# Performance work log

Measured on AMD Instinct MI355X. Metric: run time of the kernel, lower is better.

Reference implementation:

```python
import jax, jax.numpy as jnp
import numpy as np

N_SRC, N_DST, N_EDGES, E = 100000, 50000, 600000, 128

def setup_inputs() -> dict:
    key = jax.random.key(0)
    k1, k2, k3, k4, k5, k6 = jax.random.split(key, 6)
    return {
        "h_src": jax.random.normal(k1, (N_SRC, E), dtype=jnp.float32),
        "weights": jax.random.uniform(k2, (N_EDGES,), dtype=jnp.float32),
        "src_idx": jax.random.randint(k3, (N_EDGES,), 0, N_SRC, dtype=jnp.int32),
        "dst_idx": jax.random.randint(k4, (N_EDGES,), 0, N_DST, dtype=jnp.int32),
        "num_dst": N_DST,
        "q_w": jax.random.normal(k5, (E, E), dtype=jnp.float32) * (2.0 / np.sqrt(E + E)),  # xavier-ish, gain=sqrt(2)
        "q_b": jnp.zeros((E,), dtype=jnp.float32),
        "w_w": jax.random.normal(k6, (E, 2 * E), dtype=jnp.float32) * (2.0 / np.sqrt(E + 2 * E)),
        "w_b": jnp.zeros((E,), dtype=jnp.float32),
    }

def reference(h_src, weights, src_idx, dst_idx, num_dst, q_w, q_b, w_w, w_b):
    h_dst = h_src[:num_dst]                                  # [n_dst, E]
    n = jax.nn.relu(h_src @ q_w.T + q_b)                     # [n_src, E] (dropout=eval/no-op)
    w = weights.astype(jnp.float32)
    m = n[src_idx] * w[:, None]                              # [n_edges, E] edge messages
    agg = jax.ops.segment_sum(m, dst_idx, num_segments=num_dst)   # weighted feature sum
    ws = jax.ops.segment_sum(w, dst_idx, num_segments=num_dst)    # weight sum
    ws = jnp.clip(ws, 1.0, None)[:, None]                    # clamp(min=1)
    z = jnp.concatenate([h_dst, agg / ws], axis=1)           # [n_dst, 2E]
    z = jax.nn.relu(z @ w_w.T + w_b)                         # [n_dst, E]
    z_norm = jnp.linalg.norm(z, axis=1, keepdims=True)
    z_norm = jnp.where(z_norm == 0, 1.0, z_norm)
    return z / z_norm
```

## Files before the change

kernel.cpp:

```cpp
#include <hip/hip_runtime.h>
#include <math.h>


typedef __attribute__((ext_vector_type(8))) short  short8;
typedef __attribute__((ext_vector_type(8))) __bf16 bf16x8;
typedef __attribute__((ext_vector_type(4))) float  f32x4;

#define MFMA16(a, b, c) __builtin_amdgcn_mfma_f32_16x16x32_bf16( \
    __builtin_bit_cast(bf16x8, (a)), __builtin_bit_cast(bf16x8, (b)), (c), 0, 0, 0)

#define EDGE_CAP 2048

__device__ __forceinline__ ushort f2bf(float x) {
    unsigned u = __float_as_uint(x);
    return (ushort)((u + 0x7fffu + ((u >> 16) & 1u)) >> 16);
}
__device__ __forceinline__ float bfhi(unsigned p) { return __uint_as_float(p & 0xffff0000u); }
__device__ __forceinline__ float bflo(unsigned p) { return __uint_as_float(p << 16); }

__device__ __forceinline__ short8 cvt8(float4 v0, float4 v1) {
    ushort t[8] = { f2bf(v0.x), f2bf(v0.y), f2bf(v0.z), f2bf(v0.w),
                    f2bf(v1.x), f2bf(v1.y), f2bf(v1.z), f2bf(v1.w) };
    return *(short8*)t;
}

__global__ __launch_bounds__(512) void k_hist(const int* __restrict__ dst,
    int* __restrict__ hist, int nedges, int nb)
{
    __shared__ int hl[2048];
    const int g = blockIdx.x, tid = threadIdx.x, G = gridDim.x;
    for (int i = tid; i < nb; i += 512) hl[i] = 0;
    __syncthreads();
    const int chunk = (nedges + G - 1) / G;
    const int e0 = g * chunk, e1 = min(e0 + chunk, nedges);
    for (int e = e0 + tid; e < e1; e += 512)
        atomicAdd(&hl[dst[e] >> 5], 1);
    __syncthreads();
    for (int i = tid; i < nb; i += 512) hist[i * G + g] = hl[i];
}

__global__ __launch_bounds__(1024) void k_scan_blk(const int* __restrict__ counts,
    int* __restrict__ offs, int* __restrict__ partials, int n)
{
    __shared__ int wtot[16];
    const int tid = threadIdx.x, lane = tid & 63, wv = tid >> 6;
    const int idx = blockIdx.x * 1024 + tid;
    int v = (idx < n) ? counts[idx] : 0;
    int x = v;
    #pragma unroll
    for (int off = 1; off < 64; off <<= 1) {
        int y = __shfl_up(x, off);
        if (lane >= off) x += y;
    }
    if (lane == 63) wtot[wv] = x;
    __syncthreads();
    if (tid == 0) {
        int r = 0;
        #pragma unroll
        for (int q = 0; q < 16; ++q) { int t = wtot[q]; wtot[q] = r; r += t; }
    }
    __syncthreads();
    if (idx < n) offs[idx] = wtot[wv] + x - v;
    if (tid == 1023) partials[blockIdx.x] = wtot[15] + x;
}

__global__ __launch_bounds__(512) void k_part_gemm1(
    const int* __restrict__ src, const int* __restrict__ dst,
    const float* __restrict__ w, const int* __restrict__ binoff0,
    const int* __restrict__ partials, int2* __restrict__ eb,
    int nedges, int nb, int nbs, int G,
    const float* __restrict__ h, const float* __restrict__ qw,
    const float* __restrict__ qb, ushort* __restrict__ nout, int nrows)
{
    __shared__ __align__(16) ushort aL[128 * 128];
    __shared__ __align__(16) ushort bL[128 * 128];
    __shared__ int wtmp[8];
    const int tid = threadIdx.x;

    if (blockIdx.x < G) {
        int* cur   = (int*)aL;
        int* pscan = (int*)bL;
        const int g = blockIdx.x;
        {
            const int lane = tid & 63, wv = tid >> 6;
            int v = (tid < nbs) ? partials[tid] : 0;
            int x = v;
            #pragma unroll
            for (int off = 1; off < 64; off <<= 1) {
                int y = __shfl_up(x, off);
                if (lane >= off) x += y;
            }
            if (lane == 63) wtmp[wv] = x;
            __syncthreads();
            if (tid == 0) {
                int r = 0;
                #pragma unroll
                for (int q = 0; q < 4; ++q) { int t = wtmp[q]; wtmp[q] = r; r += t; }
            }
            __syncthreads();
            if (tid < nbs) pscan[tid] = wtmp[wv] + x - v;
        }
        __syncthreads();
        for (int b = tid; b < nb; b += 512) {
            int i = b * G + g;
            cur[b] = binoff0[i] + pscan[i >> 10];
        }
        __syncthreads();
        const int chunk = (nedges + G - 1) / G;
        const int e0 = g * chunk, e1 = min(e0 + chunk, nedges);
        for (int e = e0 + tid; e < e1; e += 512) {
            int d = dst[e];
            int pos = atomicAdd(&cur[d >> 5], 1);
            eb[pos] = make_int2(((d & 31) << 17) | src[e], __float_as_int(w[e]));
        }
        return;
    }

    const int rb = (blockIdx.x - G) * 128;
    const int rr = tid >> 4, sl = tid & 15;

    #pragma unroll
    for (int rg = 0; rg < 4; ++rg) {
        int row = rg * 32 + rr, gr = rb + row;
        float4 a0 = make_float4(0.f,0.f,0.f,0.f), a1 = a0;
        if (gr < nrows) {
            a0 = *(const float4*)&h[(size_t)gr * 128 + sl * 8];
            a1 = *(const float4*)&h[(size_t)gr * 128 + sl * 8 + 4];
        }
        *(short8*)&aL[row * 128 + (sl ^ (row & 7)) * 8] = cvt8(a0, a1);
        float4 b0 = *(const float4*)&qw[row * 128 + sl * 8];
        float4 b1 = *(const float4*)&qw[row * 128 + sl * 8 + 4];
        *(short8*)&bL[row * 128 + (sl ^ (row & 7)) * 8] = cvt8(b0, b1);
    }
    __syncthreads();

    const int w_ = tid >> 6, l = tid & 63;
    const int lr = l & 15, lk = l >> 4;
    const int row = w_ * 16 + lr;

    short8 a[4];
    #pragma unroll
    for (int ks = 0; ks < 4; ++ks)
        a[ks] = *(const short8*)&aL[row * 128 + ((ks * 4 + lk) ^ (lr & 7)) * 8];

    f32x4 acc[8];
    #pragma unroll
    for (int nt = 0; nt < 8; ++nt) acc[nt] = (f32x4){0.f, 0.f, 0.f, 0.f};

    #pragma unroll
    for (int nt = 0; nt < 8; ++nt)
        #pragma unroll
        for (int ks = 0; ks < 4; ++ks) {
            short8 b = *(const short8*)&bL[(nt * 16 + lr) * 128 + ((ks * 4 + lk) ^ (lr & 7)) * 8];
            acc[nt] = MFMA16(b, a[ks], acc[nt]);
        }

    const int gr = rb + row;
    if (gr < nrows) {
        #pragma unroll
        for (int nt = 0; nt < 8; ++nt) {
            float4 bv = *(const float4*)&qb[nt * 16 + lk * 4];
            ushort t[4];
            t[0] = f2bf(fmaxf(acc[nt][0] + bv.x, 0.f));
            t[1] = f2bf(fmaxf(acc[nt][1] + bv.y, 0.f));
            t[2] = f2bf(fmaxf(acc[nt][2] + bv.z, 0.f));
            t[3] = f2bf(fmaxf(acc[nt][3] + bv.w, 0.f));
            *(ushort4*)&nout[(size_t)gr * 128 + nt * 16 + lk * 4] = *(ushort4*)t;
        }
    }
}

__global__ __launch_bounds__(256) void k_bsort_gather(const ushort* __restrict__ nsrc,
    const int2* __restrict__ eb, const int* __restrict__ binoff0,
    const int* __restrict__ partials, ushort* __restrict__ z2,
    int ndst, int nedges, int G, int NB, int nbs)
{
    __shared__ int2 els[EDGE_CAP];
    __shared__ int  pscan[256];
    __shared__ int  base[33];
    __shared__ int  cur[32];
    __shared__ int  wtmp[4];
    const int b = blockIdx.x, tid = threadIdx.x;

    {
        const int lane = tid & 63, wv = tid >> 6;
        int v = (tid < nbs) ? partials[tid] : 0;
        int x = v;
        #pragma unroll
        for (int off = 1; off < 64; off <<= 1) {
            int y = __shfl_up(x, off);
            if (lane >= off) x += y;
        }
        if (lane == 63) wtmp[wv] = x;
        __syncthreads();
        if (tid == 0) {
            int r = 0;
            #pragma unroll
            for (int q = 0; q < 4; ++q) { int t = wtmp[q]; wtmp[q] = r; r += t; }
        }
        __syncthreads();
        if (tid < nbs) pscan[tid] = wtmp[wv] + x - v;
    }
    if (tid < 32) cur[tid] = 0;
    __syncthreads();

    const int i0 = b * G;
    const int j0 = binoff0[i0] + pscan[i0 >> 10];
    int j1 = nedges;
    if (b != NB - 1) {
        int i1 = (b + 1) * G;
        j1 = binoff0[i1] + pscan[i1 >> 10];
    }
    const int cnt_e = j1 - j0;

    for (int j = j0 + tid; j < j1; j += 256)
        atomicAdd(&cur[eb[j].x >> 17], 1);
    __syncthreads();

    if (tid < 64) {
        int a = (tid < 32) ? cur[tid] : 0;
        int x = a;
        #pragma unroll
        for (int off = 1; off < 64; off <<= 1) {
            int y = __shfl_up(x, off);
            if (tid >= off) x += y;
        }
        if (tid < 32) {
            base[tid] = x - a;
            cur[tid]  = x - a;
        }
        if (tid == 31) base[32] = x;
    }
    __syncthreads();

    const int wv = tid >> 6, lane = tid & 63;
    const int g = lane >> 4, s = lane & 15;

    if (cnt_e <= EDGE_CAP) {
        for (int j = j0 + tid; j < j1; j += 256) {
            int2 e = eb[j];
            int pos = atomicAdd(&cur[e.x >> 17], 1);
            els[pos] = make_int2(e.x & 0x1FFFF, e.y);
        }
        __syncthreads();

        for (int r = wv; r < 32; r += 4) {
            int gr = b * 32 + r;
            if (gr >= ndst) break;
            const int ja = base[r], jb = base[r + 1];
            float acc[8] = {0.f,0.f,0.f,0.f,0.f,0.f,0.f,0.f};
            float ws = 0.f;
            for (int j = ja + g; j < jb; j += 8) {
                int2 e1 = els[j];
                bool has2 = (j + 4 < jb);
                int2 e2 = has2 ? els[j + 4] : e1;
                float w1 = __int_as_float(e1.y);
                float w2 = has2 ? __int_as_float(e2.y) : 0.f;
                short8 r1 = *(const short8*)&nsrc[(size_t)e1.x * 128 + s * 8];
                short8 r2 = *(const short8*)&nsrc[(size_t)e2.x * 128 + s * 8];
                uint4 p1 = __builtin_bit_cast(uint4, r1);
                uint4 p2 = __builtin_bit_cast(uint4, r2);
                acc[0] = fmaf(bflo(p1.x), w1, acc[0]);
                acc[1] = fmaf(bfhi(p1.x), w1, acc[1]);
                acc[2] = fmaf(bflo(p1.y), w1, acc[2]);
                acc[3] = fmaf(bfhi(p1.y), w1, acc[3]);
                acc[4] = fmaf(bflo(p1.z), w1, acc[4]);
                acc[5] = fmaf(bfhi(p1.z), w1, acc[5]);
                acc[6] = fmaf(bflo(p1.w), w1, acc[6]);
                acc[7] = fmaf(bfhi(p1.w), w1, acc[7]);
                acc[0] = fmaf(bflo(p2.x), w2, acc[0]);
                acc[1] = fmaf(bfhi(p2.x), w2, acc[1]);
                acc[2] = fmaf(bflo(p2.y), w2, acc[2]);
                acc[3] = fmaf(bfhi(p2.y), w2, acc[3]);
                acc[4] = fmaf(bflo(p2.z), w2, acc[4]);
                acc[5] = fmaf(bfhi(p2.z), w2, acc[5]);
                acc[6] = fmaf(bflo(p2.w), w2, acc[6]);
                acc[7] = fmaf(bfhi(p2.w), w2, acc[7]);
                ws += w1 + w2;
            }
            #pragma unroll
            for (int i = 0; i < 8; ++i) {
                acc[i] += __shfl_xor(acc[i], 16);
                acc[i] += __shfl_xor(acc[i], 32);
            }
            ws += __shfl_xor(ws, 16);
            ws += __shfl_xor(ws, 32);
            if (g == 0) {
                float inv = 1.f / fmaxf(ws, 1.f);
                ushort t8[8];
                #pragma unroll
                for (int i = 0; i < 8; ++i) t8[i] = f2bf(acc[i] * inv);
                *(short8*)&z2[(size_t)gr * 128 + s * 8] = *(short8*)t8;
            }
        }
    } else {
        for (int r = wv; r < 32; r += 4) {
            int gr = b * 32 + r;
            if (gr >= ndst) break;
            float acc[8] = {0.f,0.f,0.f,0.f,0.f,0.f,0.f,0.f};
            float ws = 0.f;
            for (int j = j0 + g; j < j1; j += 4) {
                int2 e = eb[j];
                if ((e.x >> 17) != r) continue;
                float we = __int_as_float(e.y);
                short8 rv = *(const short8*)&nsrc[(size_t)(e.x & 0x1FFFF) * 128 + s * 8];
                uint4 p = __builtin_bit_cast(uint4, rv);
                acc[0] = fmaf(bflo(p.x), we, acc[0]);
                acc[1] = fmaf(bfhi(p.x), we, acc[1]);
                acc[2] = fmaf(bflo(p.y), we, acc[2]);
                acc[3] = fmaf(bfhi(p.y), we, acc[3]);
                acc[4] = fmaf(bflo(p.z), we, acc[4]);
                acc[5] = fmaf(bfhi(p.z), we, acc[5]);
                acc[6] = fmaf(bflo(p.w), we, acc[6]);
                acc[7] = fmaf(bfhi(p.w), we, acc[7]);
                ws += we;
            }
            #pragma unroll
            for (int i = 0; i < 8; ++i) {
                acc[i] += __shfl_xor(acc[i], 16);
                acc[i] += __shfl_xor(acc[i], 32);
            }
            ws += __shfl_xor(ws, 16);
            ws += __shfl_xor(ws, 32);
            if (g == 0) {
                float inv = 1.f / fmaxf(ws, 1.f);
                ushort t8[8];
                #pragma unroll
                for (int i = 0; i < 8; ++i) t8[i] = f2bf(acc[i] * inv);
                *(short8*)&z2[(size_t)gr * 128 + s * 8] = *(short8*)t8;
            }
        }
    }
}

__global__ __launch_bounds__(512) void k_gemm2(const float* __restrict__ h,
    const ushort* __restrict__ z2, const float* __restrict__ ww,
    const float* __restrict__ wb, float* __restrict__ out, int nrows)
{
    __shared__ __align__(16) ushort aL[128 * 128];
    __shared__ __align__(16) ushort bL[128 * 128];
    const int tid = threadIdx.x;
    const int rb  = blockIdx.x * 128;
    const int rr = tid >> 4, sl = tid & 15;

    const int w = tid >> 6, l = tid & 63;
    const int lr = l & 15, lk = l >> 4;
    const int row = w * 16 + lr;

    f32x4 acc[8];
    #pragma unroll
    for (int nt = 0; nt < 8; ++nt) acc[nt] = (f32x4){0.f, 0.f, 0.f, 0.f};

    #pragma unroll
    for (int ph = 0; ph < 2; ++ph) {
        if (ph) __syncthreads();
        #pragma unroll
        for (int rg = 0; rg < 4; ++rg) {
            int r2 = rg * 32 + rr, gr = rb + r2;
            short8 av = (short8){0,0,0,0,0,0,0,0};
            if (gr < nrows) {
                if (ph == 0) {
                    float4 a0 = *(const float4*)&h[(size_t)gr * 128 + sl * 8];
                    float4 a1 = *(const float4*)&h[(size_t)gr * 128 + sl * 8 + 4];
                    av = cvt8(a0, a1);
                } else {
                    av = *(const short8*)&z2[(size_t)gr * 128 + sl * 8];
                }
            }
            *(short8*)&aL[r2 * 128 + (sl ^ (r2 & 7)) * 8] = av;
            float4 b0 = *(const float4*)&ww[r2 * 256 + ph * 128 + sl * 8];
            float4 b1 = *(const float4*)&ww[r2 * 256 + ph * 128 + sl * 8 + 4];
            *(short8*)&bL[r2 * 128 + (sl ^ (r2 & 7)) * 8] = cvt8(b0, b1);
        }
        __syncthreads();

        short8 a[4];
        #pragma unroll
        for (int ks = 0; ks < 4; ++ks)
            a[ks] = *(const short8*)&aL[row * 128 + ((ks * 4 + lk) ^ (lr & 7)) * 8];

        #pragma unroll
        for (int nt = 0; nt < 8; ++nt)
            #pragma unroll
            for (int ks = 0; ks < 4; ++ks) {
                short8 b = *(const short8*)&bL[(nt * 16 + lr) * 128 + ((ks * 4 + lk) ^ (lr & 7)) * 8];
                acc[nt] = MFMA16(b, a[ks], acc[nt]);
            }
    }

    float val[8][4];
    float ss = 0.f;
    #pragma unroll
    for (int nt = 0; nt < 8; ++nt) {
        float4 bv = *(const float4*)&wb[nt * 16 + lk * 4];
        #pragma unroll
        for (int v = 0; v < 4; ++v) {
            float x = acc[nt][v] + ((const float*)&bv)[v];
            x = fmaxf(x, 0.f);
            val[nt][v] = x;
            ss = fmaf(x, x, ss);
        }
    }
    ss += __shfl_xor(ss, 16);
    ss += __shfl_xor(ss, 32);
    float nr = sqrtf(ss);
    nr = (nr == 0.f) ? 1.f : nr;
    float inv = 1.f / nr;

    const int gr = rb + row;
    if (gr < nrows) {
        #pragma unroll
        for (int nt = 0; nt < 8; ++nt) {
            float4 o;
            o.x = val[nt][0] * inv; o.y = val[nt][1] * inv;
            o.z = val[nt][2] * inv; o.w = val[nt][3] * inv;
            *(float4*)&out[(size_t)gr * 128 + nt * 16 + lk * 4] = o;
        }
    }
}

extern "C" void kernel_launch(void* const* d_in, const int* in_sizes, int n_in,
                              void* d_out, int out_size, void* d_ws, size_t ws_size,
                              hipStream_t stream)
{
    const float* h   = (const float*)d_in[0];
    const float* wts = (const float*)d_in[1];
    const int*   src = (const int*)d_in[2];
    const int*   dst = (const int*)d_in[3];
    const float* qw  = (const float*)d_in[5];
    const float* qb  = (const float*)d_in[6];
    const float* www = (const float*)d_in[7];
    const float* wb  = (const float*)d_in[8];
    float* out = (float*)d_out;

    const int n_src   = in_sizes[0] / 128;
    const int n_edges = in_sizes[1];
    const int n_dst   = out_size / 128;

    const int G  = 128;
    const int NB = (n_dst + 31) / 32;
    const int NBINS = NB * G;
    const int nbs = (NBINS + 1023) / 1024;

    ushort* nbuf    = (ushort*)d_ws;
    ushort* z2      = nbuf + (size_t)n_src * 128;
    int2*   eb      = (int2*)(z2 + (size_t)n_dst * 128);
    int*    hist    = (int*)(eb + n_edges);
    int*    binoff0 = hist + NBINS;
    int*    parts   = binoff0 + NBINS;

    k_hist<<<G, 512, 0, stream>>>(dst, hist, n_edges, NB);

    k_scan_blk<<<nbs, 1024, 0, stream>>>(hist, binoff0, parts, NBINS);

    const int t1 = (n_src + 127) / 128;
    k_part_gemm1<<<G + t1, 512, 0, stream>>>(src, dst, wts, binoff0, parts, eb,
                                             n_edges, NB, nbs, G,
                                             h, qw, qb, nbuf, n_src);

    k_bsort_gather<<<NB, 256, 0, stream>>>(nbuf, eb, binoff0, parts, z2,
                                           n_dst, n_edges, G, NB, nbs);

    const int t2 = (n_dst + 127) / 128;
    k_gemm2<<<t2, 512, 0, stream>>>(h, z2, www, wb, out, n_dst);
}
```

Baseline: 86.56 us.

## Process two row tiles per GEMM1 block with register prefetch of next tile

The GEMM1 part of the fused partition/GEMM kernel now launches half as many tile blocks, and each block handles two 128-row tiles. The q_w weight tile is converted into shared memory once and reused for both tiles, and the next tile's h rows are prefetched into registers while the current tile's MFMAs run. This amortizes the weight load and conversion and hides global load latency. In exchange it adds register pressure from 8 float4 prefetch registers and leaves fewer blocks, which may reduce occupancy and parallelism across CUs.

```diff
diff --git a/kernel.cpp b/kernel.cpp
--- a/kernel.cpp
+++ b/kernel.cpp
@@ -70,7 +70,8 @@
     const int* __restrict__ partials, int2* __restrict__ eb,
     int nedges, int nb, int nbs, int G,
     const float* __restrict__ h, const float* __restrict__ qw,
-    const float* __restrict__ qb, ushort* __restrict__ nout, int nrows)
+    const float* __restrict__ qb, ushort* __restrict__ nout,
+    int nrows, int t1, int NT2)
 {
     __shared__ __align__(16) ushort aL[128 * 128];
     __shared__ __align__(16) ushort bL[128 * 128];
@@ -116,56 +117,93 @@
         return;
     }
 
-    const int rb = (blockIdx.x - G) * 128;
+    const int gb = blockIdx.x - G;
     const int rr = tid >> 4, sl = tid & 15;
 
     #pragma unroll
     for (int rg = 0; rg < 4; ++rg) {
-        int row = rg * 32 + rr, gr = rb + row;
-        float4 a0 = make_float4(0.f,0.f,0.f,0.f), a1 = a0;
-        if (gr < nrows) {
-            a0 = *(const float4*)&h[(size_t)gr * 128 + sl * 8];
-            a1 = *(const float4*)&h[(size_t)gr * 128 + sl * 8 + 4];
-        }
-        *(short8*)&aL[row * 128 + (sl ^ (row & 7)) * 8] = cvt8(a0, a1);
+        int row = rg * 32 + rr;
         float4 b0 = *(const float4*)&qw[row * 128 + sl * 8];
         float4 b1 = *(const float4*)&qw[row * 128 + sl * 8 + 4];
         *(short8*)&bL[row * 128 + (sl ^ (row & 7)) * 8] = cvt8(b0, b1);
     }
-    __syncthreads();
 
     const int w_ = tid >> 6, l = tid & 63;
     const int lr = l & 15, lk = l >> 4;
     const int row = w_ * 16 + lr;
 
-    short8 a[4];
-    #pragma unroll
-    for (int ks = 0; ks < 4; ++ks)
-        a[ks] = *(const short8*)&aL[row * 128 + ((ks * 4 + lk) ^ (lr & 7)) * 8];
-
-    f32x4 acc[8];
-    #pragma unroll
-    for (int nt = 0; nt < 8; ++nt) acc[nt] = (f32x4){0.f, 0.f, 0.f, 0.f};
-
-    #pragma unroll
-    for (int nt = 0; nt < 8; ++nt)
-        #pragma unroll
-        for (int ks = 0; ks < 4; ++ks) {
-            short8 b = *(const short8*)&bL[(nt * 16 + lr) * 128 + ((ks * 4 + lk) ^ (lr & 7)) * 8];
-            acc[nt] = MFMA16(b, a[ks], acc[nt]);
-        }
-
-    const int gr = rb + row;
-    if (gr < nrows) {
-        #pragma unroll
-        for (int nt = 0; nt < 8; ++nt) {
-            float4 bv = *(const float4*)&qb[nt * 16 + lk * 4];
-            ushort t[4];
-            t[0] = f2bf(fmaxf(acc[nt][0] + bv.x, 0.f));
-            t[1] = f2bf(fmaxf(acc[nt][1] + bv.y, 0.f));
-            t[2] = f2bf(fmaxf(acc[nt][2] + bv.z, 0.f));
-            t[3] = f2bf(fmaxf(acc[nt][3] + bv.w, 0.f));
-            *(ushort4*)&nout[(size_t)gr * 128 + nt * 16 + lk * 4] = *(ushort4*)t;
+    float4 pa[8];
+    {
+        const int rb = gb * 128;
+        #pragma unroll
+        for (int rg = 0; rg < 4; ++rg) {
+            int gr = rb + rg * 32 + rr;
+            if (gr < nrows) {
+                pa[rg*2]   = *(const float4*)&h[(size_t)gr * 128 + sl * 8];
+                pa[rg*2+1] = *(const float4*)&h[(size_t)gr * 128 + sl * 8 + 4];
+            } else {
+                pa[rg*2] = pa[rg*2+1] = make_float4(0.f,0.f,0.f,0.f);
+            }
+        }
+    }
+
+    for (int it = 0; it < 2; ++it) {
+        const int tt = gb + it * NT2;
+        if (tt >= t1) break;
+        const int rb = tt * 128;
+
+        __syncthreads();
+        #pragma unroll
+        for (int rg = 0; rg < 4; ++rg) {
+            int r2 = rg * 32 + rr;
+            *(short8*)&aL[r2 * 128 + (sl ^ (r2 & 7)) * 8] = cvt8(pa[rg*2], pa[rg*2+1]);
+        }
+        __syncthreads();
+
+        const int tn = gb + (it + 1) * NT2;
+        if (tn < t1) {
+            const int rbn = tn * 128;
+            #pragma unroll
+            for (int rg = 0; rg < 4; ++rg) {
+                int gr = rbn + rg * 32 + rr;
+                if (gr < nrows) {
+                    pa[rg*2]   = *(const float4*)&h[(size_t)gr * 128 + sl * 8];
+                    pa[rg*2+1] = *(const float4*)&h[(size_t)gr * 128 + sl * 8 + 4];
+                } else {
+                    pa[rg*2] = pa[rg*2+1] = make_float4(0.f,0.f,0.f,0.f);
+                }
+            }
+        }
+
+        short8 a[4];
+        #pragma unroll
+        for (int ks = 0; ks < 4; ++ks)
+            a[ks] = *(const short8*)&aL[row * 128 + ((ks * 4 + lk) ^ (lr & 7)) * 8];
+
+        f32x4 acc[8];
+        #pragma unroll
+        for (int nt = 0; nt < 8; ++nt) acc[nt] = (f32x4){0.f, 0.f, 0.f, 0.f};
+
+        #pragma unroll
+        for (int nt = 0; nt < 8; ++nt)
+            #pragma unroll
+            for (int ks = 0; ks < 4; ++ks) {
+                short8 b = *(const short8*)&bL[(nt * 16 + lr) * 128 + ((ks * 4 + lk) ^ (lr & 7)) * 8];
+                acc[nt] = MFMA16(b, a[ks], acc[nt]);
+            }
+
+        const int gr = rb + row;
+        if (gr < nrows) {
+            #pragma unroll
+            for (int nt = 0; nt < 8; ++nt) {
+                float4 bv = *(const float4*)&qb[nt * 16 + lk * 4];
+                ushort t[4];
+                t[0] = f2bf(fmaxf(acc[nt][0] + bv.x, 0.f));
+                t[1] = f2bf(fmaxf(acc[nt][1] + bv.y, 0.f));
+                t[2] = f2bf(fmaxf(acc[nt][2] + bv.z, 0.f));
+                t[3] = f2bf(fmaxf(acc[nt][3] + bv.w, 0.f));
+                *(ushort4*)&nout[(size_t)gr * 128 + nt * 16 + lk * 4] = *(ushort4*)t;
+            }
         }
     }
 }
@@ -453,10 +491,11 @@
 
     k_scan_blk<<<nbs, 1024, 0, stream>>>(hist, binoff0, parts, NBINS);
 
-    const int t1 = (n_src + 127) / 128;
-    k_part_gemm1<<<G + t1, 512, 0, stream>>>(src, dst, wts, binoff0, parts, eb,
-                                             n_edges, NB, nbs, G,
-                                             h, qw, qb, nbuf, n_src);
+    const int t1  = (n_src + 127) / 128;
+    const int NT2 = (t1 + 1) / 2;
+    k_part_gemm1<<<G + NT2, 512, 0, stream>>>(src, dst, wts, binoff0, parts, eb,
+                                              n_edges, NB, nbs, G,
+                                              h, qw, qb, nbuf, n_src, t1, NT2);
 
     k_bsort_gather<<<NB, 256, 0, stream>>>(nbuf, eb, binoff0, parts, z2,
                                            n_dst, n_edges, G, NB, nbs);
```

After: 86.51 us. Within noise of the previous version (-0.1%).

## Pre-convert inputs to bf16 and stage GEMM tiles with direct global-to-LDS loads

Applied to the files above, without the earlier changes.

Extra blocks in the histogram kernel convert h_src, q_w and w_w from fp32 to bf16 once, writing them into new workspace buffers. Both GEMM kernels then fill their LDS tiles with global_load_lds 16-byte transfers from those buffers, instead of loading fp32 into registers, converting and storing to LDS. The aim is to cut per-tile conversion work and register round-trips and to hide the conversion behind the histogram pass. In exchange it adds a full extra read and write of h_src, which raises total memory traffic. It also drops the row bounds checks on the last tile, so that tile reads past the end of each buffer into neighbouring workspace memory.

```diff
diff --git a/kernel.cpp b/kernel.cpp
--- a/kernel.cpp
+++ b/kernel.cpp
@@ -24,11 +24,37 @@
     return *(short8*)t;
 }
 
-__global__ __launch_bounds__(512) void k_hist(const int* __restrict__ dst,
-    int* __restrict__ hist, int nedges, int nb)
-{
+__device__ __forceinline__ void gload16(const void* g, void* l) {
+    __builtin_amdgcn_global_load_lds(
+        (const __attribute__((address_space(1))) void*)g,
+        (__attribute__((address_space(3))) void*)l, 16, 0, 0);
+}
+
+__global__ __launch_bounds__(512) void k_hist_cvt(const int* __restrict__ dst,
+    int* __restrict__ hist, int nedges, int nb, int G,
+    const float* __restrict__ h, const float* __restrict__ qw,
+    const float* __restrict__ ww, ushort* __restrict__ hb,
+    ushort* __restrict__ qwb, ushort* __restrict__ wwb, int n_src)
+{
+    const int tid = threadIdx.x;
+    if ((int)blockIdx.x >= G) {
+        const long Uh = (long)n_src * 16;
+        const long Uq = 2048, Uw = 4096;
+        const long u0 = (long)(blockIdx.x - G) * 512 + tid;
+        const long stride = (long)(gridDim.x - G) * 512;
+        for (long u = u0; u < Uh + Uq + Uw; u += stride) {
+            const float* s; ushort* d; long i;
+            if (u < Uh)            { s = h;  d = hb;  i = u; }
+            else if (u < Uh + Uq)  { s = qw; d = qwb; i = u - Uh; }
+            else                   { s = ww; d = wwb; i = u - Uh - Uq; }
+            float4 a0 = *(const float4*)&s[i * 8];
+            float4 a1 = *(const float4*)&s[i * 8 + 4];
+            *(short8*)&d[i * 8] = cvt8(a0, a1);
+        }
+        return;
+    }
     __shared__ int hl[2048];
-    const int g = blockIdx.x, tid = threadIdx.x, G = gridDim.x;
+    const int g = blockIdx.x;
     for (int i = tid; i < nb; i += 512) hl[i] = 0;
     __syncthreads();
     const int chunk = (nedges + G - 1) / G;
@@ -69,7 +95,7 @@
     const float* __restrict__ w, const int* __restrict__ binoff0,
     const int* __restrict__ partials, int2* __restrict__ eb,
     int nedges, int nb, int nbs, int G,
-    const float* __restrict__ h, const float* __restrict__ qw,
+    const ushort* __restrict__ hb, const ushort* __restrict__ qwb,
     const float* __restrict__ qb, ushort* __restrict__ nout, int nrows)
 {
     __shared__ __align__(16) ushort aL[128 * 128];
@@ -77,7 +103,7 @@
     __shared__ int wtmp[8];
     const int tid = threadIdx.x;
 
-    if (blockIdx.x < G) {
+    if ((int)blockIdx.x < G) {
         int* cur   = (int*)aL;
         int* pscan = (int*)bL;
         const int g = blockIdx.x;
@@ -116,27 +142,20 @@
         return;
     }
 
-    const int rb = (blockIdx.x - G) * 128;
-    const int rr = tid >> 4, sl = tid & 15;
-
-    #pragma unroll
-    for (int rg = 0; rg < 4; ++rg) {
-        int row = rg * 32 + rr, gr = rb + row;
-        float4 a0 = make_float4(0.f,0.f,0.f,0.f), a1 = a0;
-        if (gr < nrows) {
-            a0 = *(const float4*)&h[(size_t)gr * 128 + sl * 8];
-            a1 = *(const float4*)&h[(size_t)gr * 128 + sl * 8 + 4];
-        }
-        *(short8*)&aL[row * 128 + (sl ^ (row & 7)) * 8] = cvt8(a0, a1);
-        float4 b0 = *(const float4*)&qw[row * 128 + sl * 8];
-        float4 b1 = *(const float4*)&qw[row * 128 + sl * 8 + 4];
-        *(short8*)&bL[row * 128 + (sl ^ (row & 7)) * 8] = cvt8(b0, b1);
-    }
-    __syncthreads();
-
+    const int gb = blockIdx.x - G;
+    const int rb = gb * 128;
     const int w_ = tid >> 6, l = tid & 63;
     const int lr = l & 15, lk = l >> 4;
     const int row = w_ * 16 + lr;
+
+    #pragma unroll
+    for (int i = 0; i < 4; ++i) {
+        const int rl   = w_ * 16 + i * 4 + (l >> 4);
+        const int slot = (l & 15) ^ (rl & 7);
+        gload16(&qwb[rl * 128 + slot * 8],                 &bL[(w_ * 16 + i * 4) * 128]);
+        gload16(&hb[(size_t)(rb + rl) * 128 + slot * 8],   &aL[(w_ * 16 + i * 4) * 128]);
+    }
+    __syncthreads();
 
     short8 a[4];
     #pragma unroll
@@ -333,15 +352,14 @@
     }
 }
 
-__global__ __launch_bounds__(512) void k_gemm2(const float* __restrict__ h,
-    const ushort* __restrict__ z2, const float* __restrict__ ww,
+__global__ __launch_bounds__(512) void k_gemm2(const ushort* __restrict__ hb,
+    const ushort* __restrict__ z2, const ushort* __restrict__ wwb,
     const float* __restrict__ wb, float* __restrict__ out, int nrows)
 {
     __shared__ __align__(16) ushort aL[128 * 128];
     __shared__ __align__(16) ushort bL[128 * 128];
     const int tid = threadIdx.x;
     const int rb  = blockIdx.x * 128;
-    const int rr = tid >> 4, sl = tid & 15;
 
     const int w = tid >> 6, l = tid & 63;
     const int lr = l & 15, lk = l >> 4;
@@ -354,23 +372,13 @@
     #pragma unroll
     for (int ph = 0; ph < 2; ++ph) {
         if (ph) __syncthreads();
-        #pragma unroll
-        for (int rg = 0; rg < 4; ++rg) {
-            int r2 = rg * 32 + rr, gr = rb + r2;
-            short8 av = (short8){0,0,0,0,0,0,0,0};
-            if (gr < nrows) {
-                if (ph == 0) {
-                    float4 a0 = *(const float4*)&h[(size_t)gr * 128 + sl * 8];
-                    float4 a1 = *(const float4*)&h[(size_t)gr * 128 + sl * 8 + 4];
-                    av = cvt8(a0, a1);
-                } else {
-                    av = *(const short8*)&z2[(size_t)gr * 128 + sl * 8];
-                }
-            }
-            *(short8*)&aL[r2 * 128 + (sl ^ (r2 & 7)) * 8] = av;
-            float4 b0 = *(const float4*)&ww[r2 * 256 + ph * 128 + sl * 8];
-            float4 b1 = *(const float4*)&ww[r2 * 256 + ph * 128 + sl * 8 + 4];
-            *(short8*)&bL[r2 * 128 + (sl ^ (r2 & 7)) * 8] = cvt8(b0, b1);
+        const ushort* As = ph ? z2 : hb;
+        #pragma unroll
+        for (int i = 0; i < 4; ++i) {
+            const int rl   = w * 16 + i * 4 + (l >> 4);
+            const int slot = (l & 15) ^ (rl & 7);
+            gload16(&wwb[rl * 256 + ph * 128 + slot * 8],     &bL[(w * 16 + i * 4) * 128]);
+            gload16(&As[(size_t)(rb + rl) * 128 + slot * 8],  &aL[(w * 16 + i * 4) * 128]);
         }
         __syncthreads();
 
@@ -444,23 +452,28 @@
 
     ushort* nbuf    = (ushort*)d_ws;
     ushort* z2      = nbuf + (size_t)n_src * 128;
-    int2*   eb      = (int2*)(z2 + (size_t)n_dst * 128);
+    ushort* hb      = z2 + (size_t)n_dst * 128;
+    ushort* qwb     = hb + (size_t)n_src * 128;
+    ushort* wwb     = qwb + 16384;
+    int2*   eb      = (int2*)(wwb + 32768);
     int*    hist    = (int*)(eb + n_edges);
     int*    binoff0 = hist + NBINS;
     int*    parts   = binoff0 + NBINS;
 
-    k_hist<<<G, 512, 0, stream>>>(dst, hist, n_edges, NB);
+    const int CVT = 768;
+    k_hist_cvt<<<G + CVT, 512, 0, stream>>>(dst, hist, n_edges, NB, G,
+                                            h, qw, www, hb, qwb, wwb, n_src);
 
     k_scan_blk<<<nbs, 1024, 0, stream>>>(hist, binoff0, parts, NBINS);
 
     const int t1 = (n_src + 127) / 128;
     k_part_gemm1<<<G + t1, 512, 0, stream>>>(src, dst, wts, binoff0, parts, eb,
                                              n_edges, NB, nbs, G,
-                                             h, qw, qb, nbuf, n_src);
+                                             hb, qwb, qb, nbuf, n_src);
 
     k_bsort_gather<<<NB, 256, 0, stream>>>(nbuf, eb, binoff0, parts, z2,
                                            n_dst, n_edges, G, NB, nbs);
 
     const int t2 = (n_dst + 127) / 128;
-    k_gemm2<<<t2, 512, 0, stream>>>(h, z2, www, wb, out, n_dst);
-}
+    k_gemm2<<<t2, 512, 0, stream>>>(hb, z2, wwb, wb, out, n_dst);
+}
```

Measured after the change: 84.02 us, median of 2. -2.9%, faster.
